# Kernel tuning notes

Hardware: AMD Instinct MI355X
Metric: run time of the kernel (lower is better)

## Reference

```python
import jax, jax.numpy as jnp
import numpy as np

INPUT_DIM = 256
OUTPUT_DIM = 256
GRID_SIZE = 32


def setup_inputs() -> dict:
    key = jax.random.key(0)
    k1, k2 = jax.random.split(key)
    x = jax.random.normal(k1, (4096, INPUT_DIM), dtype=jnp.float32)
    # fouriercoeffs: randn(2, out, in, grid) / (sqrt(in) * sqrt(grid))  (smooth_initialization=False)
    scale = np.sqrt(INPUT_DIM) * np.sqrt(GRID_SIZE)
    fouriercoeffs = jax.random.normal(k2, (2, OUTPUT_DIM, INPUT_DIM, GRID_SIZE), dtype=jnp.float32) / scale
    bias = jnp.zeros((1, OUTPUT_DIM), dtype=jnp.float32)
    return {"x": x, "fouriercoeffs": fouriercoeffs, "bias": bias}


def reference(x, fouriercoeffs, bias):
    # x: [N, input_dim]; fouriercoeffs: [2, out, in, grid]; bias: [1, out]
    grid_size = fouriercoeffs.shape[-1]
    k = jnp.arange(1, grid_size + 1, dtype=x.dtype)  # [grid]
    phase = x[:, :, None] * k  # [N, in, grid]
    c = jnp.cos(phase)
    s = jnp.sin(phase)
    # contraction over (in, grid) -> GEMM-like einsum; same math as the
    # original broadcast-multiply-sum but without the [N,out,in,grid] blowup
    y = jnp.einsum("big,jig->bj", c, fouriercoeffs[0])
    y = y + jnp.einsum("big,jig->bj", s, fouriercoeffs[1])
    y = y + bias
    return y
```

## Files before the change

kernel.cpp:

```cpp
#include <hip/hip_runtime.h>
#include <hip/hip_bf16.h>
#include <cstdint>

typedef __attribute__((ext_vector_type(8))) short  short8;
typedef __attribute__((ext_vector_type(4))) float  f32x4;
typedef __attribute__((ext_vector_type(4))) unsigned uint4v;

#define N_ROWS   4096
#define IN_DIM   256
#define OUT_DIM  256
#define K_TOTAL  16384
#define SPLITK   8
#define KCHUNK   2048
#define BM       128
#define BN       128
#define BK       64
#define STEPS    32

__global__ void convert_coeffs(const float* __restrict__ w,
                               __hip_bfloat16* __restrict__ bm) {
    int gid = blockIdx.x * 256 + threadIdx.x;
    int j = gid >> 14;
    int k = gid & (K_TOTAL - 1);
    int i = k >> 6;
    int r = k & 63;
    int g = r >> 1;
    int p = r & 1;
    float v = w[(((p << 8) + j) * 256 + i) * 32 + g];
    bm[gid] = __float2bfloat16(v);
}

__global__ void bias_fill(const float* __restrict__ bias, float* __restrict__ out) {
    int gid = blockIdx.x * 256 + threadIdx.x;
    out[gid] = bias[gid & (OUT_DIM - 1)];
}

__device__ __forceinline__ void gld_lds16(const void* g, void* l) {
    __builtin_amdgcn_global_load_lds(
        (const __attribute__((address_space(1))) void*)(uintptr_t)g,
        (__attribute__((address_space(3))) void*)(uintptr_t)l, 16, 0, 0);
}

__device__ __forceinline__ unsigned f2bf(float f) {
    unsigned u = __builtin_bit_cast(unsigned, f);
    return (u + 0x7fffu + ((u >> 16) & 1u)) >> 16;
}

__global__ __launch_bounds__(256, 2) void fkan_gemm(const float* __restrict__ x,
                                                    const __hip_bfloat16* __restrict__ bm,
                                                    float* __restrict__ out) {
    __shared__ float  x_lds[STEPS][BM];
    __shared__ short  A_lds[BM * BK];
    __shared__ short  B_lds[2][BN * BK];

    const int tid  = threadIdx.x;
    const int lane = tid & 63;
    const int wid  = tid >> 6;
    const int wm   = wid >> 1;
    const int wn   = wid & 1;

    const int bid = blockIdx.x;
    const int ks  = bid & 7;
    const int tt  = bid >> 3;
    const int mb  = tt >> 1;
    const int nb  = tt & 1;
    const int m0  = mb * BM;
    const int n0  = nb * BN;
    const int i0  = ks * STEPS;
    const int kbase = ks * KCHUNK;

    auto stage_B = [&](int s, int buf) {
        int kg = kbase + s * BK;
        #pragma unroll
        for (int r = 0; r < 4; ++r) {
            int jl = wid * 32 + r * 8 + (lane >> 3);
            int cg = (lane & 7) ^ (jl & 7);
            const __hip_bfloat16* src = bm + (size_t)(n0 + jl) * K_TOTAL + kg + cg * 8;
            gld_lds16(src, &B_lds[buf][(wid * 32 + r * 8) * BK]);
        }
    };

    const int am = tid & 127;
    const int ah = tid >> 7;

    auto gen_A = [&](int s) {
        float xv = x_lds[s][am];
        float c1, s1; __sincosf(xv, &s1, &c1);
        float cg, sg; __sincosf((float)(16 * ah + 1) * xv, &sg, &cg);
        unsigned pk[16];
        #pragma unroll
        for (int e = 0; e < 16; ++e) {
            pk[e] = f2bf(cg) | (f2bf(sg) << 16);
            float cn = cg * c1 - sg * s1;
            sg = sg * c1 + cg * s1;
            cg = cn;
        }
        int base = am * BK;
        #pragma unroll
        for (int q = 0; q < 4; ++q) {
            uint4v w = {pk[4 * q], pk[4 * q + 1], pk[4 * q + 2], pk[4 * q + 3]};
            *(uint4v*)&A_lds[base + (((4 * ah + q) ^ (am & 7)) << 3)] = w;
        }
    };

    f32x4 acc[4][4];
    #pragma unroll
    for (int a = 0; a < 4; ++a)
        #pragma unroll
        for (int b = 0; b < 4; ++b) acc[a][b] = (f32x4){0.f, 0.f, 0.f, 0.f};

    auto compute = [&](int buf) {
        const int rA = lane & 15;
        const int cA = lane >> 4;
        #pragma unroll
        for (int kf = 0; kf < 2; ++kf) {
            short8 af[4], bf[4];
            #pragma unroll
            for (int mf = 0; mf < 4; ++mf) {
                int row = wm * 64 + mf * 16 + rA;
                int ch  = (kf * 4 + cA) ^ (rA & 7);
                af[mf] = *(const short8*)&A_lds[row * BK + ch * 8];
            }
            #pragma unroll
            for (int nf = 0; nf < 4; ++nf) {
                int row = wn * 64 + nf * 16 + rA;
                int ch  = (kf * 4 + cA) ^ (rA & 7);
                bf[nf] = *(const short8*)&B_lds[buf][row * BK + ch * 8];
            }
            #pragma unroll
            for (int mf = 0; mf < 4; ++mf)
                #pragma unroll
                for (int nf = 0; nf < 4; ++nf)
                    acc[mf][nf] = __builtin_amdgcn_mfma_f32_16x16x32_bf16(
                        af[mf], bf[nf], acc[mf][nf], 0, 0, 0);
        }
    };

    stage_B(0, 0);
    #pragma unroll
    for (int s2 = 0; s2 < 4; ++s2) {
        int slot = tid + s2 * 256;
        int m  = slot >> 3;
        int c4 = slot & 7;
        f32x4 xv = *(const f32x4*)&x[(size_t)(m0 + m) * IN_DIM + i0 + c4 * 4];
        #pragma unroll
        for (int q = 0; q < 4; ++q) x_lds[c4 * 4 + q][m] = xv[q];
    }
    __syncthreads();
    gen_A(0);

    int cur = 0;
    for (int s = 0; s < STEPS; ++s) {
        __syncthreads();
        if (s + 1 < STEPS) stage_B(s + 1, cur ^ 1);
        compute(cur);
        __syncthreads();
        if (s + 1 < STEPS) gen_A(s + 1);
        cur ^= 1;
    }

    const int cl = lane & 15;
    const int rl = (lane >> 4) * 4;
    #pragma unroll
    for (int mf = 0; mf < 4; ++mf) {
        #pragma unroll
        for (int nf = 0; nf < 4; ++nf) {
            int row = m0 + wm * 64 + mf * 16 + rl;
            int col = n0 + wn * 64 + nf * 16 + cl;
            #pragma unroll
            for (int r2 = 0; r2 < 4; ++r2)
                atomicAdd(&out[(size_t)(row + r2) * OUT_DIM + col], acc[mf][nf][r2]);
        }
    }
}

extern "C" void kernel_launch(void* const* d_in, const int* in_sizes, int n_in,
                              void* d_out, int out_size, void* d_ws, size_t ws_size,
                              hipStream_t stream) {
    const float* x      = (const float*)d_in[0];
    const float* coeffs = (const float*)d_in[1];
    const float* bias   = (const float*)d_in[2];
    float* out = (float*)d_out;
    __hip_bfloat16* bmat = (__hip_bfloat16*)d_ws;

    convert_coeffs<<<(OUT_DIM * K_TOTAL) / 256, 256, 0, stream>>>(coeffs, bmat);
    bias_fill<<<(N_ROWS * OUT_DIM) / 256, 256, 0, stream>>>(bias, out);
    fkan_gemm<<<SPLITK * (N_ROWS / BM) * (OUT_DIM / BN), 256, 0, stream>>>(x, bmat, out);
}
```

Baseline: 144.0 us.

## Replace split-K atomics with partial buffers plus reduce; vectorize coefficient conversion

The GEMM kernel now writes each split-K slice's partial tile to a separate workspace buffer with plain stores. A new reduce kernel sums the eight partials and adds the bias, which replaces the bias_fill and atomicAdd path when the workspace is large enough. The coefficient conversion kernel also switches from one scattered scalar read per element to vector loads of four floats from each of the cos and sin planes, packed into one 16-byte store. This removes atomic contention and the bias prefill, but adds about 32 MB of partial writes and reads plus an extra launch.

```diff
diff --git a/kernel.cpp b/kernel.cpp
--- a/kernel.cpp
+++ b/kernel.cpp
@@ -17,22 +17,45 @@
 #define BK       64
 #define STEPS    32
 
+#define BMAT_BYTES   (OUT_DIM * K_TOTAL * 2)
+#define PART_ELEMS   (N_ROWS * OUT_DIM)
+#define WS_NEEDED    (BMAT_BYTES + SPLITK * PART_ELEMS * 4)
+
 __global__ void convert_coeffs(const float* __restrict__ w,
                                __hip_bfloat16* __restrict__ bm) {
     int gid = blockIdx.x * 256 + threadIdx.x;
-    int j = gid >> 14;
-    int k = gid & (K_TOTAL - 1);
-    int i = k >> 6;
-    int r = k & 63;
-    int g = r >> 1;
-    int p = r & 1;
-    float v = w[(((p << 8) + j) * 256 + i) * 32 + g];
-    bm[gid] = __float2bfloat16(v);
+    int j   = gid >> 11;
+    int rem = gid & 2047;
+    int i   = rem >> 3;
+    int g4  = rem & 7;
+    const float* s0 = w + ((size_t)(j * 256 + i)) * 32 + g4 * 4;
+    const float* s1 = s0 + (size_t)OUT_DIM * IN_DIM * 32;
+    f32x4 c4 = *(const f32x4*)s0;
+    f32x4 sn = *(const f32x4*)s1;
+    __hip_bfloat16 o[8];
+    #pragma unroll
+    for (int q = 0; q < 4; ++q) {
+        o[2 * q]     = __float2bfloat16(c4[q]);
+        o[2 * q + 1] = __float2bfloat16(sn[q]);
+    }
+    *(short8*)(bm + (size_t)j * K_TOTAL + i * 64 + g4 * 8) = *(short8*)o;
 }
 
 __global__ void bias_fill(const float* __restrict__ bias, float* __restrict__ out) {
     int gid = blockIdx.x * 256 + threadIdx.x;
     out[gid] = bias[gid & (OUT_DIM - 1)];
+}
+
+__global__ void reduce_out(const float* __restrict__ part,
+                           const float* __restrict__ bias,
+                           float* __restrict__ out) {
+    int gid = blockIdx.x * 256 + threadIdx.x;
+    int idx = gid * 4;
+    f32x4 a = *(const f32x4*)&bias[idx & (OUT_DIM - 1)];
+    #pragma unroll
+    for (int ks = 0; ks < SPLITK; ++ks)
+        a += *(const f32x4*)&part[(size_t)ks * PART_ELEMS + idx];
+    *(f32x4*)&out[idx] = a;
 }
 
 __device__ __forceinline__ void gld_lds16(const void* g, void* l) {
@@ -46,9 +69,10 @@
     return (u + 0x7fffu + ((u >> 16) & 1u)) >> 16;
 }
 
+template <bool PART>
 __global__ __launch_bounds__(256, 2) void fkan_gemm(const float* __restrict__ x,
                                                     const __hip_bfloat16* __restrict__ bm,
-                                                    float* __restrict__ out) {
+                                                    float* __restrict__ dst) {
     __shared__ float  x_lds[STEPS][BM];
     __shared__ short  A_lds[BM * BK];
     __shared__ short  B_lds[2][BN * BK];
@@ -161,6 +185,7 @@
 
     const int cl = lane & 15;
     const int rl = (lane >> 4) * 4;
+    float* base = PART ? dst + (size_t)ks * PART_ELEMS : dst;
     #pragma unroll
     for (int mf = 0; mf < 4; ++mf) {
         #pragma unroll
@@ -168,8 +193,12 @@
             int row = m0 + wm * 64 + mf * 16 + rl;
             int col = n0 + wn * 64 + nf * 16 + cl;
             #pragma unroll
-            for (int r2 = 0; r2 < 4; ++r2)
-                atomicAdd(&out[(size_t)(row + r2) * OUT_DIM + col], acc[mf][nf][r2]);
+            for (int r2 = 0; r2 < 4; ++r2) {
+                if (PART)
+                    base[(size_t)(row + r2) * OUT_DIM + col] = acc[mf][nf][r2];
+                else
+                    atomicAdd(&base[(size_t)(row + r2) * OUT_DIM + col], acc[mf][nf][r2]);
+            }
         }
     }
 }
@@ -182,8 +211,16 @@
     const float* bias   = (const float*)d_in[2];
     float* out = (float*)d_out;
     __hip_bfloat16* bmat = (__hip_bfloat16*)d_ws;
-
-    convert_coeffs<<<(OUT_DIM * K_TOTAL) / 256, 256, 0, stream>>>(coeffs, bmat);
-    bias_fill<<<(N_ROWS * OUT_DIM) / 256, 256, 0, stream>>>(bias, out);
-    fkan_gemm<<<SPLITK * (N_ROWS / BM) * (OUT_DIM / BN), 256, 0, stream>>>(x, bmat, out);
-}
+    float* part = (float*)((char*)d_ws + BMAT_BYTES);
+
+    convert_coeffs<<<(OUT_DIM * IN_DIM * 8) / 256, 256, 0, stream>>>(coeffs, bmat);
+
+    const int grid = SPLITK * (N_ROWS / BM) * (OUT_DIM / BN);
+    if (ws_size >= (size_t)WS_NEEDED) {
+        fkan_gemm<true><<<grid, 256, 0, stream>>>(x, bmat, part);
+        reduce_out<<<PART_ELEMS / 4 / 256, 256, 0, stream>>>(part, bias, out);
+    } else {
+        bias_fill<<<(N_ROWS * OUT_DIM) / 256, 256, 0, stream>>>(bias, out);
+        fkan_gemm<false><<<grid, 256, 0, stream>>>(x, bmat, out);
+    }
+}
```

Measured after the change: 127.8 us. -11.2%, faster.
